# Optimization experiments

Measured on AMD Instinct MI355X. Metric: run time of the kernel, lower is better.

Reference implementation:

```python
import jax, jax.numpy as jnp
import numpy as np

N = 100_000      # nodes
E1 = 1_600_000   # masked_x edges
E2 = 400_000     # y edges
IN = 128         # in_channels
LAT = 32         # latent_size


def setup_inputs() -> dict:
    key = jax.random.key(0)
    k1, k2, k3, k4 = jax.random.split(key, 4)
    x = jax.random.normal(k1, (N, IN), dtype=jnp.float32)
    edge_index = jax.random.randint(k2, (2, E1), 0, N, dtype=jnp.int64)
    y_edge_index = jax.random.randint(k3, (2, E2), 0, N, dtype=jnp.int64)
    # GCNConv linear weight [IN, LAT] (glorot-ish scale) and bias [LAT]
    W = jax.random.normal(k4, (IN, LAT), dtype=jnp.float32) * (1.0 / np.sqrt(IN))
    b = jnp.zeros((LAT,), dtype=jnp.float32)
    return {"x": x, "edge_index": edge_index, "y_edge_index": y_edge_index, "W": W, "b": b}


def reference(x, edge_index, y_edge_index, W, b):
    n = x.shape[0]
    # Encoder2: concat edge indices, then GCNConv(x, combined_edge_index)
    ei = jnp.concatenate([edge_index, y_edge_index], axis=1)
    # GCNConv: add self-loops
    loops = jnp.arange(n, dtype=ei.dtype)
    src = jnp.concatenate([ei[0], loops])  # message sources
    dst = jnp.concatenate([ei[1], loops])  # aggregation targets
    # symmetric degree normalization deg^{-1/2}[src] * deg^{-1/2}[dst]
    deg = jax.ops.segment_sum(jnp.ones(src.shape, dtype=x.dtype), dst, num_segments=n)
    dinv = jax.lax.rsqrt(jnp.where(deg > 0, deg, 1.0))
    norm = dinv[src] * dinv[dst]  # [E_total]
    # linear transform first (smaller latent dim => cheaper gather/scatter)
    h = x @ W  # [N, LAT]
    msgs = h[src] * norm[:, None]  # gather + normalize, [E_total, LAT]
    out = jax.ops.segment_sum(msgs, dst, num_segments=n) + b  # scatter-add + bias
    return out
```

## Files before the change

### kernel.cpp

```cpp
#include <hip/hip_runtime.h>
#include <hip/hip_bf16.h>


#define LATD 32
#define INCH 128
#define BSH 7
#define BW 128
#define CAP 4096
#define ACH 4096

typedef short bf16x8 __attribute__((ext_vector_type(8)));
typedef float f32x4 __attribute__((ext_vector_type(4)));

__device__ __forceinline__ short f2bf(float f) {
    __hip_bfloat16 t = __float2bfloat16(f);
    return *(short*)&t;
}

__device__ __forceinline__ void lds_fadd(float* p, float v) {
    unsigned off = (unsigned)(unsigned long long)p;
    asm volatile("ds_add_f32 %0, %1" :: "v"(off), "v"(v) : "memory");
}

__device__ __forceinline__ void load_edge(const int* __restrict__ ei, const int* __restrict__ yei,
                                          int e1, int e2, int e, int& src, int& dst) {
    if (e < e1) { src = ei[e]; dst = ei[e1 + e]; }
    else        { int t = e - e1; src = yei[t]; dst = yei[e2 + t]; }
}

__global__ void prep_k(const float* __restrict__ W, __hip_bfloat16* __restrict__ Wf,
                       int* __restrict__ bcursor) {
    int i = blockIdx.x * 256 + threadIdx.x;
    if (i < 1024) bcursor[i] = 0;
    int e = i - 1024;
    if (e >= 0 && e < INCH * LATD) {
        int k = e >> 5, c = e & 31;
        Wf[((k >> 3) * 32 + c) * 8 + (k & 7)] = __float2bfloat16(W[e]);
    }
}

__global__ __launch_bounds__(512) void gemm_fused_k(const float* __restrict__ x,
                                                    const __hip_bfloat16* __restrict__ Wf,
                                                    __hip_bfloat16* __restrict__ h,
                                                    const unsigned* __restrict__ bucketed,
                                                    const int* __restrict__ bcursor,
                                                    int* __restrict__ deg, int n) {
    __shared__ int cnt[BW];
    int tid = threadIdx.x;
    int b = blockIdx.x;
    int row0 = b << BSH;
    if (bucketed) {
        if (tid < BW) cnt[tid] = 0;
        __syncthreads();
        size_t s = (size_t)b * CAP;
        int tot = bcursor[b]; if (tot > CAP) tot = CAP;
        for (int i = tid; i < tot; i += 512)
            atomicAdd(&cnt[bucketed[s + i] & (BW - 1)], 1);
        __syncthreads();
        if (tid < BW) {
            int node = row0 + tid;
            if (node < n) deg[node] = cnt[tid];
        }
    }
    int lane = tid & 63, wv = tid >> 6;
    int r = lane & 15, g = lane >> 4;
    int grow = row0 + (wv << 4) + r;
    bool rok = grow < n;
    const float* xrow = x + (size_t)grow * INCH + g * 8;
    const short* Wfb = (const short*)Wf;
    f32x4 acc0 = {0.f, 0.f, 0.f, 0.f};
    f32x4 acc1 = {0.f, 0.f, 0.f, 0.f};
#pragma unroll
    for (int s = 0; s < 4; ++s) {
        bf16x8 af = {};
        if (rok) {
            float4 a0 = *(const float4*)(xrow + s * 32);
            float4 a1 = *(const float4*)(xrow + s * 32 + 4);
            af[0] = f2bf(a0.x); af[1] = f2bf(a0.y); af[2] = f2bf(a0.z); af[3] = f2bf(a0.w);
            af[4] = f2bf(a1.x); af[5] = f2bf(a1.y); af[6] = f2bf(a1.z); af[7] = f2bf(a1.w);
        }
        bf16x8 bf0 = *(const bf16x8*)(Wfb + (size_t)(((s * 4 + g) * 32) + r) * 8);
        bf16x8 bf1 = *(const bf16x8*)(Wfb + (size_t)(((s * 4 + g) * 32) + r + 16) * 8);
        acc0 = __builtin_amdgcn_mfma_f32_16x16x32_bf16(af, bf0, acc0, 0, 0, 0);
        acc1 = __builtin_amdgcn_mfma_f32_16x16x32_bf16(af, bf1, acc1, 0, 0, 0);
    }
#pragma unroll
    for (int i = 0; i < 4; ++i) {
        int rl = (wv << 4) + (g << 2) + i;
        int gr = row0 + rl;
        if (gr < n) {
            float dv = bucketed ? rsqrtf((float)cnt[rl] + 1.0f) : 1.0f;
            h[(size_t)gr * LATD + r]      = __float2bfloat16(acc0[i] * dv);
            h[(size_t)gr * LATD + r + 16] = __float2bfloat16(acc1[i] * dv);
        }
    }
}

__global__ void zero_i32_k(int* p, int cnt) {
    int i = blockIdx.x * 256 + threadIdx.x;
    if (i < cnt) p[i] = 0;
}

__global__ __launch_bounds__(512) void passA_scatter_k(const int* __restrict__ ei, const int* __restrict__ yei,
                                                       int e1, int e2, int* __restrict__ bcursor,
                                                       unsigned* __restrict__ bucketed, int NB) {
    __shared__ int hist[1024];
    __shared__ int scanex[1024];
    __shared__ int segb[1024];
    __shared__ int wsum[8], wbase[8];
    __shared__ unsigned raw[ACH];
    __shared__ unsigned short rawb[ACH];
    __shared__ unsigned stage[ACH];
    __shared__ unsigned short bof[ACH];
    int tid = threadIdx.x;
    int E = e1 + e2;
    int e0 = blockIdx.x * ACH;
    int m = E - e0; if (m > ACH) m = ACH;
    for (int i = tid; i < 1024; i += 512) hist[i] = 0;
    __syncthreads();
    for (int i = tid; i < m; i += 512) {
        int src, dst; load_edge(ei, yei, e1, e2, e0 + i, src, dst);
        int b = dst >> BSH;
        raw[i]  = ((unsigned)src << BSH) | (unsigned)(dst & (BW - 1));
        rawb[i] = (unsigned short)b;
        atomicAdd(&hist[b], 1);
    }
    __syncthreads();
    int b2i = tid * 2;
    int c0 = hist[b2i], c1 = hist[b2i + 1];
    int pair = c0 + c1;
    int lane = tid & 63, wv = tid >> 6;
    int incl = pair;
#pragma unroll
    for (int off = 1; off < 64; off <<= 1) {
        int t = __shfl_up(incl, off);
        if (lane >= off) incl += t;
    }
    if (lane == 63) wsum[wv] = incl;
    __syncthreads();
    if (tid < 8) {
        int v = wsum[tid];
        int inc2 = v;
#pragma unroll
        for (int off = 1; off < 8; off <<= 1) {
            int t = __shfl_up(inc2, off);
            if (tid >= off) inc2 += t;
        }
        wbase[tid] = inc2 - v;
    }
    __syncthreads();
    int excl = wbase[wv] + incl - pair;
    scanex[b2i] = excl; scanex[b2i + 1] = excl + c0;
    __syncthreads();
    for (int b = tid; b < NB; b += 512)
        segb[b] = hist[b] ? atomicAdd(&bcursor[b], hist[b]) : 0;
    __syncthreads();
    for (int b = tid; b < 1024; b += 512) hist[b] = scanex[b];
    __syncthreads();
    for (int i = tid; i < m; i += 512) {
        unsigned pk = raw[i]; int b = rawb[i];
        int pos = atomicAdd(&hist[b], 1);
        stage[pos] = pk;
        bof[pos] = (unsigned short)b;
    }
    __syncthreads();
    for (int i = tid; i < m; i += 512) {
        int b = bof[i];
        int pos = segb[b] + (i - scanex[b]);
        if (pos < CAP)
            bucketed[(size_t)b * CAP + pos] = stage[i];
    }
}

__global__ __launch_bounds__(512) void passB2_k(const unsigned* __restrict__ bucketed,
                                                const int* __restrict__ bcursor,
                                                const int* __restrict__ deg,
                                                const __hip_bfloat16* __restrict__ hs,
                                                const float* __restrict__ bias,
                                                float* __restrict__ out, int n) {
    __shared__ unsigned sorted[CAP];
    __shared__ float oacc[BW][LATD];
    __shared__ int cnt[BW], cur[BW];
    int tid = threadIdx.x;
    int b = blockIdx.x;
    size_t s = (size_t)b * CAP;
    int tot = bcursor[b]; if (tot > CAP) tot = CAP;
    int dst0 = b << BSH;
    unsigned ereg[8];
#pragma unroll
    for (int k = 0; k < 8; ++k) {
        int i = tid + (k << 9);
        ereg[k] = (i < tot) ? bucketed[s + i] : 0xFFFFFFFFu;
    }
    if (tid < BW) {
        int node = dst0 + tid;
        cnt[tid] = (node < n) ? deg[node] : 0;
    }
    for (int i = tid; i < BW * LATD; i += 512) ((float*)oacc)[i] = 0.f;
    __syncthreads();
    if (tid < 64) {
        int b2 = tid * 2;
        int c0 = cnt[b2], c1 = cnt[b2 + 1];
        int pair = c0 + c1;
        int incl = pair;
#pragma unroll
        for (int off = 1; off < 64; off <<= 1) {
            int t = __shfl_up(incl, off);
            if (tid >= off) incl += t;
        }
        int excl = incl - pair;
        cur[b2] = excl; cur[b2 + 1] = excl + c0;
    }
    __syncthreads();
#pragma unroll
    for (int k = 0; k < 8; ++k) {
        unsigned e = ereg[k];
        if (e != 0xFFFFFFFFu) {
            int p = atomicAdd(&cur[e & (BW - 1)], 1);
            if (p < CAP) sorted[p] = e;
        }
    }
    __syncthreads();
    const uint2* hsv = (const uint2*)hs;
    int g = tid >> 3, j4 = tid & 7;
    int span = (((tot + 63) >> 6) + 15) & ~15;
    int gs = g * span;
    int ge = gs + span; if (ge > tot) ge = tot;
    if (gs < tot) {
        float a0 = 0.f, a1 = 0.f, a2 = 0.f, a3 = 0.f;
        int cur_ld = -1;
        for (int base = gs; base < ge; base += 16) {
            int mm = ge - base; if (mm > 16) mm = 16;
            if (mm == 16) {
                unsigned pk16[16]; uint2 v16[16];
#pragma unroll
                for (int t = 0; t < 16; ++t) {
                    pk16[t] = sorted[base + t];
                    v16[t] = hsv[(size_t)(pk16[t] >> BSH) * 8 + j4];
                }
#pragma unroll
                for (int t = 0; t < 16; ++t) {
                    int ld = (int)(pk16[t] & (BW - 1));
                    if (ld != cur_ld) {
                        if (cur_ld >= 0) {
                            lds_fadd(&oacc[cur_ld][j4 * 4 + 0], a0);
                            lds_fadd(&oacc[cur_ld][j4 * 4 + 1], a1);
                            lds_fadd(&oacc[cur_ld][j4 * 4 + 2], a2);
                            lds_fadd(&oacc[cur_ld][j4 * 4 + 3], a3);
                        }
                        cur_ld = ld; a0 = a1 = a2 = a3 = 0.f;
                    }
                    __hip_bfloat162 p0 = *(__hip_bfloat162*)&v16[t].x;
                    __hip_bfloat162 p1 = *(__hip_bfloat162*)&v16[t].y;
                    float2 f0 = __bfloat1622float2(p0);
                    float2 f1 = __bfloat1622float2(p1);
                    a0 += f0.x; a1 += f0.y; a2 += f1.x; a3 += f1.y;
                }
            } else {
#pragma unroll 4
                for (int t = 0; t < mm; ++t) {
                    unsigned pk = sorted[base + t];
                    uint2 v = hsv[(size_t)(pk >> BSH) * 8 + j4];
                    int ld = (int)(pk & (BW - 1));
                    if (ld != cur_ld) {
                        if (cur_ld >= 0) {
                            lds_fadd(&oacc[cur_ld][j4 * 4 + 0], a0);
                            lds_fadd(&oacc[cur_ld][j4 * 4 + 1], a1);
                            lds_fadd(&oacc[cur_ld][j4 * 4 + 2], a2);
                            lds_fadd(&oacc[cur_ld][j4 * 4 + 3], a3);
                        }
                        cur_ld = ld; a0 = a1 = a2 = a3 = 0.f;
                    }
                    __hip_bfloat162 p0 = *(__hip_bfloat162*)&v.x;
                    __hip_bfloat162 p1 = *(__hip_bfloat162*)&v.y;
                    float2 f0 = __bfloat1622float2(p0);
                    float2 f1 = __bfloat1622float2(p1);
                    a0 += f0.x; a1 += f0.y; a2 += f1.x; a3 += f1.y;
                }
            }
        }
        if (cur_ld >= 0) {
            lds_fadd(&oacc[cur_ld][j4 * 4 + 0], a0);
            lds_fadd(&oacc[cur_ld][j4 * 4 + 1], a1);
            lds_fadd(&oacc[cur_ld][j4 * 4 + 2], a2);
            lds_fadd(&oacc[cur_ld][j4 * 4 + 3], a3);
        }
    }
    __syncthreads();
    for (int idx = tid; idx < BW * (LATD / 4); idx += 512) {
        int ld = idx >> 3, q = idx & 7;
        int node = dst0 + ld;
        if (node >= n) continue;
        float dv = rsqrtf((float)cnt[ld] + 1.0f);
        int j0 = q * 4;
        ushort4 u = *(const ushort4*)&hs[(size_t)node * LATD + j0];
        float4 bv = *(const float4*)&bias[j0];
        float4 o;
        o.x = (oacc[ld][j0 + 0] + __bfloat162float(*(const __hip_bfloat16*)&u.x)) * dv + bv.x;
        o.y = (oacc[ld][j0 + 1] + __bfloat162float(*(const __hip_bfloat16*)&u.y)) * dv + bv.y;
        o.z = (oacc[ld][j0 + 2] + __bfloat162float(*(const __hip_bfloat16*)&u.z)) * dv + bv.z;
        o.w = (oacc[ld][j0 + 3] + __bfloat162float(*(const __hip_bfloat16*)&u.w)) * dv + bv.w;
        *(float4*)&out[(size_t)node * LATD + j0] = o;
    }
}

__global__ void count_k(const int* __restrict__ ei, const int* __restrict__ yei,
                        int* __restrict__ cnt, int e1, int e2) {
    int e = blockIdx.x * 256 + threadIdx.x;
    if (e >= e1 + e2) return;
    int src, dst; load_edge(ei, yei, e1, e2, e, src, dst);
    atomicAdd(&cnt[dst], 1);
}

__global__ void dinv_k(const int* __restrict__ cnt, float* __restrict__ dinv, int n) {
    int i = blockIdx.x * 256 + threadIdx.x;
    if (i < n) dinv[i] = rsqrtf((float)cnt[i] + 1.0f);
}

__global__ void selfbias_k(const float* __restrict__ dinv, const __hip_bfloat16* __restrict__ h,
                           const float* __restrict__ b, float* __restrict__ out, int total) {
    int idx = blockIdx.x * 256 + threadIdx.x;
    if (idx >= total) return;
    int i = idx >> 5, j = idx & 31;
    float d = dinv[i];
    out[idx] = __bfloat162float(h[idx]) * d * d + b[j];
}

__global__ void scatter_atomic_k(const int* __restrict__ ei, const int* __restrict__ yei,
                                 const float* __restrict__ dinv, const __hip_bfloat16* __restrict__ h,
                                 float* __restrict__ out, int e1, int e2) {
    int idx = blockIdx.x * 256 + threadIdx.x;
    int e = idx >> 5;
    if (e >= e1 + e2) return;
    int j = idx & 31;
    int src, dst; load_edge(ei, yei, e1, e2, e, src, dst);
    float norm = dinv[src] * dinv[dst];
    atomicAdd(&out[(size_t)dst * LATD + j], __bfloat162float(h[(size_t)src * LATD + j]) * norm);
}

static inline size_t aln(size_t x) { return (x + 255) & ~(size_t)255; }

extern "C" void kernel_launch(void* const* d_in, const int* in_sizes, int n_in,
                              void* d_out, int out_size, void* d_ws, size_t ws_size,
                              hipStream_t stream) {
    const float* x  = (const float*)d_in[0];
    const int* ei   = (const int*)d_in[1];
    const int* yei  = (const int*)d_in[2];
    const float* W  = (const float*)d_in[3];
    const float* b  = (const float*)d_in[4];
    float* out = (float*)d_out;

    int n  = in_sizes[0] / INCH;
    int e1 = in_sizes[1] / 2;
    int e2 = in_sizes[2] / 2;
    int E  = e1 + e2;
    int NB = (n + BW - 1) >> BSH;

    char* p = (char*)d_ws;
    size_t off = 0;
    float* dinv = (float*)(p + off);            off += aln((size_t)n * 4);
    __hip_bfloat16* h = (__hip_bfloat16*)(p + off); off += aln((size_t)n * LATD * 2);
    unsigned* bucketed = (unsigned*)(p + off);  size_t bucketed_off = off; off += aln((size_t)NB * CAP * 4);
    int* bcursor = (int*)(p + off);             off += aln((size_t)(1024 + n) * 4);
    int* deg = bcursor + 1024;
    __hip_bfloat16* Wf = (__hip_bfloat16*)(p + off); off += aln((size_t)INCH * LATD * 2);
    bool fast_ok = (off <= ws_size) && (NB <= 1024);

    if (fast_ok) {
        int ablocks = (E + ACH - 1) / ACH;
        prep_k<<<20, 256, 0, stream>>>(W, Wf, bcursor);
        passA_scatter_k<<<ablocks, 512, 0, stream>>>(ei, yei, e1, e2, bcursor, bucketed, NB);
        gemm_fused_k<<<NB, 512, 0, stream>>>(x, Wf, h, bucketed, bcursor, deg, n);
        passB2_k<<<NB, 512, 0, stream>>>(bucketed, bcursor, deg, h, b, out, n);
    } else {
        prep_k<<<20, 256, 0, stream>>>(W, Wf, bcursor);
        gemm_fused_k<<<(n + 127) / 128, 512, 0, stream>>>(x, Wf, h, nullptr, nullptr, nullptr, n);
        int* cntf = (int*)(p + bucketed_off);
        zero_i32_k<<<(n + 255) / 256, 256, 0, stream>>>(cntf, n);
        count_k<<<(E + 255) / 256, 256, 0, stream>>>(ei, yei, cntf, e1, e2);
        dinv_k<<<(n + 255) / 256, 256, 0, stream>>>(cntf, dinv, n);
        selfbias_k<<<(out_size + 255) / 256, 256, 0, stream>>>(dinv, h, b, out, out_size);
        scatter_atomic_k<<<((size_t)E * LATD + 255) / 256, 256, 0, stream>>>(ei, yei, dinv, h, out, e1, e2);
    }
}
```

Measured before the change: 166.6 us.

## Assign each 8-lane group whole destination nodes, dropping the LDS atomic accumulator

The aggregation phase of passB2 is restructured so each 8-lane group owns two destination nodes. It reads each node's contiguous run of sorted edges and keeps the partial sums in registers, then writes the normalized output directly. This removes the shared-memory accumulator, its zeroing, the ds_add_f32 atomics and the final sync and epilogue pass. The cost is load imbalance, since groups now do work proportional to their nodes' degrees instead of equal edge spans. The CAP bound check on sorted writes was also removed, which could overflow if a bucket exceeds capacity.

```diff
diff --git a/kernel.cpp b/kernel.cpp
--- a/kernel.cpp
+++ b/kernel.cpp
@@ -15,11 +15,6 @@
 __device__ __forceinline__ short f2bf(float f) {
     __hip_bfloat16 t = __float2bfloat16(f);
     return *(short*)&t;
-}
-
-__device__ __forceinline__ void lds_fadd(float* p, float v) {
-    unsigned off = (unsigned)(unsigned long long)p;
-    asm volatile("ds_add_f32 %0, %1" :: "v"(off), "v"(v) : "memory");
 }
 
 __device__ __forceinline__ void load_edge(const int* __restrict__ ei, const int* __restrict__ yei,
@@ -179,8 +174,7 @@
                                                 const float* __restrict__ bias,
                                                 float* __restrict__ out, int n) {
     __shared__ unsigned sorted[CAP];
-    __shared__ float oacc[BW][LATD];
-    __shared__ int cnt[BW], cur[BW];
+    __shared__ int cnt[BW], beg[BW], cur[BW];
     int tid = threadIdx.x;
     int b = blockIdx.x;
     size_t s = (size_t)b * CAP;
@@ -196,7 +190,6 @@
         int node = dst0 + tid;
         cnt[tid] = (node < n) ? deg[node] : 0;
     }
-    for (int i = tid; i < BW * LATD; i += 512) ((float*)oacc)[i] = 0.f;
     __syncthreads();
     if (tid < 64) {
         int b2 = tid * 2;
@@ -209,7 +202,8 @@
             if (tid >= off) incl += t;
         }
         int excl = incl - pair;
-        cur[b2] = excl; cur[b2 + 1] = excl + c0;
+        beg[b2] = excl;      beg[b2 + 1] = excl + c0;
+        cur[b2] = excl;      cur[b2 + 1] = excl + c0;
     }
     __syncthreads();
 #pragma unroll
@@ -217,90 +211,60 @@
         unsigned e = ereg[k];
         if (e != 0xFFFFFFFFu) {
             int p = atomicAdd(&cur[e & (BW - 1)], 1);
-            if (p < CAP) sorted[p] = e;
+            sorted[p] = e;
         }
     }
     __syncthreads();
     const uint2* hsv = (const uint2*)hs;
     int g = tid >> 3, j4 = tid & 7;
-    int span = (((tot + 63) >> 6) + 15) & ~15;
-    int gs = g * span;
-    int ge = gs + span; if (ge > tot) ge = tot;
-    if (gs < tot) {
+#pragma unroll
+    for (int q = 0; q < 2; ++q) {
+        int nd = 2 * g + q;
+        int node = dst0 + nd;
+        int beg_ = beg[nd];
+        int cnt_ = cnt[nd];
         float a0 = 0.f, a1 = 0.f, a2 = 0.f, a3 = 0.f;
-        int cur_ld = -1;
-        for (int base = gs; base < ge; base += 16) {
-            int mm = ge - base; if (mm > 16) mm = 16;
-            if (mm == 16) {
-                unsigned pk16[16]; uint2 v16[16];
-#pragma unroll
-                for (int t = 0; t < 16; ++t) {
-                    pk16[t] = sorted[base + t];
-                    v16[t] = hsv[(size_t)(pk16[t] >> BSH) * 8 + j4];
-                }
-#pragma unroll
-                for (int t = 0; t < 16; ++t) {
-                    int ld = (int)(pk16[t] & (BW - 1));
-                    if (ld != cur_ld) {
-                        if (cur_ld >= 0) {
-                            lds_fadd(&oacc[cur_ld][j4 * 4 + 0], a0);
-                            lds_fadd(&oacc[cur_ld][j4 * 4 + 1], a1);
-                            lds_fadd(&oacc[cur_ld][j4 * 4 + 2], a2);
-                            lds_fadd(&oacc[cur_ld][j4 * 4 + 3], a3);
-                        }
-                        cur_ld = ld; a0 = a1 = a2 = a3 = 0.f;
-                    }
-                    __hip_bfloat162 p0 = *(__hip_bfloat162*)&v16[t].x;
-                    __hip_bfloat162 p1 = *(__hip_bfloat162*)&v16[t].y;
-                    float2 f0 = __bfloat1622float2(p0);
-                    float2 f1 = __bfloat1622float2(p1);
-                    a0 += f0.x; a1 += f0.y; a2 += f1.x; a3 += f1.y;
-                }
-            } else {
+        int i = 0;
+        for (; i + 8 <= cnt_; i += 8) {
+            unsigned pk8[8]; uint2 v8[8];
+#pragma unroll
+            for (int t = 0; t < 8; ++t) pk8[t] = sorted[beg_ + i + t];
+#pragma unroll
+            for (int t = 0; t < 8; ++t) v8[t] = hsv[(size_t)(pk8[t] >> BSH) * 8 + j4];
+#pragma unroll
+            for (int t = 0; t < 8; ++t) {
+                __hip_bfloat162 p0 = *(__hip_bfloat162*)&v8[t].x;
+                __hip_bfloat162 p1 = *(__hip_bfloat162*)&v8[t].y;
+                float2 f0 = __bfloat1622float2(p0);
+                float2 f1 = __bfloat1622float2(p1);
+                a0 += f0.x; a1 += f0.y; a2 += f1.x; a3 += f1.y;
+            }
+        }
 #pragma unroll 4
-                for (int t = 0; t < mm; ++t) {
-                    unsigned pk = sorted[base + t];
-                    uint2 v = hsv[(size_t)(pk >> BSH) * 8 + j4];
-                    int ld = (int)(pk & (BW - 1));
-                    if (ld != cur_ld) {
-                        if (cur_ld >= 0) {
-                            lds_fadd(&oacc[cur_ld][j4 * 4 + 0], a0);
-                            lds_fadd(&oacc[cur_ld][j4 * 4 + 1], a1);
-                            lds_fadd(&oacc[cur_ld][j4 * 4 + 2], a2);
-                            lds_fadd(&oacc[cur_ld][j4 * 4 + 3], a3);
-                        }
-                        cur_ld = ld; a0 = a1 = a2 = a3 = 0.f;
-                    }
-                    __hip_bfloat162 p0 = *(__hip_bfloat162*)&v.x;
-                    __hip_bfloat162 p1 = *(__hip_bfloat162*)&v.y;
-                    float2 f0 = __bfloat1622float2(p0);
-                    float2 f1 = __bfloat1622float2(p1);
-                    a0 += f0.x; a1 += f0.y; a2 += f1.x; a3 += f1.y;
-                }
-            }
-        }
-        if (cur_ld >= 0) {
-            lds_fadd(&oacc[cur_ld][j4 * 4 + 0], a0);
-            lds_fadd(&oacc[cur_ld][j4 * 4 + 1], a1);
-            lds_fadd(&oacc[cur_ld][j4 * 4 + 2], a2);
-            lds_fadd(&oacc[cur_ld][j4 * 4 + 3], a3);
-        }
-    }
-    __syncthreads();
-    for (int idx = tid; idx < BW * (LATD / 4); idx += 512) {
-        int ld = idx >> 3, q = idx & 7;
-        int node = dst0 + ld;
-        if (node >= n) continue;
-        float dv = rsqrtf((float)cnt[ld] + 1.0f);
-        int j0 = q * 4;
-        ushort4 u = *(const ushort4*)&hs[(size_t)node * LATD + j0];
-        float4 bv = *(const float4*)&bias[j0];
-        float4 o;
-        o.x = (oacc[ld][j0 + 0] + __bfloat162float(*(const __hip_bfloat16*)&u.x)) * dv + bv.x;
-        o.y = (oacc[ld][j0 + 1] + __bfloat162float(*(const __hip_bfloat16*)&u.y)) * dv + bv.y;
-        o.z = (oacc[ld][j0 + 2] + __bfloat162float(*(const __hip_bfloat16*)&u.z)) * dv + bv.z;
-        o.w = (oacc[ld][j0 + 3] + __bfloat162float(*(const __hip_bfloat16*)&u.w)) * dv + bv.w;
-        *(float4*)&out[(size_t)node * LATD + j0] = o;
+        for (; i < cnt_; ++i) {
+            unsigned pk = sorted[beg_ + i];
+            uint2 v = hsv[(size_t)(pk >> BSH) * 8 + j4];
+            __hip_bfloat162 p0 = *(__hip_bfloat162*)&v.x;
+            __hip_bfloat162 p1 = *(__hip_bfloat162*)&v.y;
+            float2 f0 = __bfloat1622float2(p0);
+            float2 f1 = __bfloat1622float2(p1);
+            a0 += f0.x; a1 += f0.y; a2 += f1.x; a3 += f1.y;
+        }
+        if (node < n) {
+            float dv = rsqrtf((float)cnt_ + 1.0f);
+            uint2 sv = hsv[(size_t)node * 8 + j4];
+            __hip_bfloat162 s0 = *(__hip_bfloat162*)&sv.x;
+            __hip_bfloat162 s1 = *(__hip_bfloat162*)&sv.y;
+            float2 sf0 = __bfloat1622float2(s0);
+            float2 sf1 = __bfloat1622float2(s1);
+            float4 bv = *(const float4*)&bias[j4 * 4];
+            float4 o;
+            o.x = (a0 + sf0.x) * dv + bv.x;
+            o.y = (a1 + sf0.y) * dv + bv.y;
+            o.z = (a2 + sf1.x) * dv + bv.z;
+            o.w = (a3 + sf1.y) * dv + bv.w;
+            *(float4*)&out[(size_t)node * LATD + j4 * 4] = o;
+        }
     }
 }
 
```

Result: faster. 154.5 us (-7.3%).
